# Optimization experiments

Measured on AMD Instinct MI355X. Metric: run time of the kernel, lower is better.

## Reference

```python
import jax, jax.numpy as jnp
import numpy as np

B, S, H, UNITS = 32, 2048, 1024, 1024


def setup_inputs() -> dict:
    key = jax.random.key(0)
    ks = jax.random.split(key, 5)
    scale = 1.0 / np.sqrt(H)
    return {
        "query": jax.random.normal(ks[0], (B, H), dtype=jnp.float32),
        "values": jax.random.normal(ks[1], (B, S, H), dtype=jnp.float32),
        "W1": jax.random.normal(ks[2], (H, UNITS), dtype=jnp.float32) * scale,
        "b1": jnp.zeros((UNITS,), dtype=jnp.float32),
        "W2": jax.random.normal(ks[3], (H, UNITS), dtype=jnp.float32) * scale,
        "b2": jnp.zeros((UNITS,), dtype=jnp.float32),
        "V": jax.random.normal(ks[4], (UNITS, 1), dtype=jnp.float32) * (1.0 / np.sqrt(UNITS)),
        "bV": jnp.zeros((1,), dtype=jnp.float32),
    }


def reference(query, values, W1, b1, W2, b2, V, bV):
    # W1(values): [B,S,U]; W2(query): [B,1,U] broadcast over S
    proj_v = jnp.einsum("bsh,hu->bsu", values, W1) + b1
    proj_q = (query @ W2 + b2)[:, None, :]
    score = jnp.tanh(proj_v + proj_q) @ V + bV          # [B,S,1]
    attention_weights = jax.nn.softmax(score, axis=1)   # softmax over seq
    context_vector = jnp.sum(attention_weights * values, axis=1)  # [B,H]
    return (attention_weights, context_vector)
```

## Files before the change

### kernel.cpp

```cpp
#include <hip/hip_runtime.h>
#include <hip/hip_bf16.h>
#include <stdint.h>

#define B_ 32
#define S_ 2048
#define H_ 1024
#define U_ 1024

typedef __attribute__((ext_vector_type(8))) short short8;
typedef __attribute__((ext_vector_type(4))) float f32x4;

#define AS1 __attribute__((address_space(1)))
#define AS3 __attribute__((address_space(3)))
#define FENCE __builtin_amdgcn_sched_barrier(0)

__device__ __forceinline__ unsigned short f2bf(float f) {
  unsigned int u = __float_as_uint(f);
  u += 0x7fffu + ((u >> 16) & 1u);
  return (unsigned short)(u >> 16);
}

__global__ void k_transpose_w1(const float* __restrict__ W1, unsigned short* __restrict__ W1T) {
  __shared__ float tile[64][65];
  const int tx = threadIdx.x, ty = threadIdx.y;
  const int u0 = blockIdx.x * 64, h0 = blockIdx.y * 64;
#pragma unroll
  for (int i = 0; i < 16; ++i) {
    int hl = ty + i * 4;
    tile[hl][tx] = W1[(size_t)(h0 + hl) * U_ + (u0 + tx)];
  }
  __syncthreads();
#pragma unroll
  for (int i = 0; i < 16; ++i) {
    int ul = ty + i * 4;
    W1T[(size_t)(u0 + ul) * H_ + (h0 + tx)] = f2bf(tile[tx][ul]);
  }
}

__global__ void k_b1q_part(const float* __restrict__ query, const float* __restrict__ W2,
                           float* __restrict__ qpart) {
  __shared__ float q_sh[32 * 128];
  const int u = blockIdx.x * 256 + threadIdx.x;
  const int hs = blockIdx.y;
  for (int i = threadIdx.x; i < 4096; i += 256) {
    const int b = i >> 7, h = i & 127;
    q_sh[i] = query[b * H_ + hs * 128 + h];
  }
  __syncthreads();
  float acc[32];
#pragma unroll
  for (int b = 0; b < 32; ++b) acc[b] = 0.f;
  for (int h = 0; h < 128; ++h) {
    const float w = W2[(size_t)(hs * 128 + h) * U_ + u];
#pragma unroll
    for (int b = 0; b < 32; ++b) acc[b] += q_sh[b * 128 + h] * w;
  }
#pragma unroll
  for (int b = 0; b < 32; ++b) qpart[((size_t)hs * 32 + b) * U_ + u] = acc[b];
}

__global__ void k_b1q_comb(const float* __restrict__ qpart, const float* __restrict__ b1,
                           const float* __restrict__ b2, float* __restrict__ b1q) {
  const int u = blockIdx.x * 256 + threadIdx.x;
  const int b = blockIdx.y;
  float s = b1[u] + b2[u];
#pragma unroll
  for (int hs = 0; hs < 8; ++hs) s += qpart[((size_t)hs * 32 + b) * U_ + u];
  b1q[b * U_ + u] = s;
}

#define BM 128
#define BN 256
#define BK 32
#define NSTEP 32

__global__ __launch_bounds__(512, 4)
void k_fused_score(const float* __restrict__ values,
                   const unsigned short* __restrict__ W1T,
                   const float* __restrict__ b1q, const float* __restrict__ V,
                   float* __restrict__ score_part) {
  __shared__ __align__(16) unsigned char smem[65536];
  unsigned short* As = (unsigned short*)smem;
  unsigned short* Bs = (unsigned short*)(smem + 16384);
  float* scorebuf = (float*)smem;

  const int tid = threadIdx.x;
  const int g = blockIdx.x;
  const int seq = (g & 7) * 256 + (g >> 3);
  const int bn = seq & 3;
  const int bm = seq >> 2;

  const int lane = tid & 63, wid = tid >> 6;
  const int wm = wid >> 2, wn = wid & 3;
  const int u0 = bn * BN;

  const int arow = tid >> 2;
  const int alc  = tid & 3;
  const int aplc = alc ^ ((arow >> 1) & 3);
  const float* aSrcF = values + (size_t)(bm * BM + arow) * H_ + alc * 8;
  const int awoff = arow * 32 + aplc * 8;

  const int blc = (tid & 3) ^ ((arow >> 1) & 3);
  const unsigned short* bSrc0 = W1T + (size_t)(u0 + arow) * H_ + blc * 8;
  const unsigned short* bSrc1 = bSrc0 + (size_t)128 * H_;

  const int l15 = lane & 15, l16 = lane >> 4;
  const int fsq = ((l16 ^ ((lane >> 1) & 3)) << 3);
  const int pA = (wm * 64 + l15) * 32 + fsq;
  const int pB = (wn * 64 + l15) * 32 + fsq;

  f32x4 acc[4][4];
#pragma unroll
  for (int mf = 0; mf < 4; ++mf)
#pragma unroll
    for (int nf = 0; nf < 4; ++nf) acc[mf][nf] = (f32x4){0.f, 0.f, 0.f, 0.f};

  float4 ar0, ar1;

#define ISSUE_ARF(tt) { \
    const float4* p_ = (const float4*)(aSrcF + (tt) * BK); \
    ar0 = p_[0]; ar1 = p_[1]; }

#define WRITE_ARF(slot) { \
    short8 w_; \
    w_[0]=f2bf(ar0.x); w_[1]=f2bf(ar0.y); w_[2]=f2bf(ar0.z); w_[3]=f2bf(ar0.w); \
    w_[4]=f2bf(ar1.x); w_[5]=f2bf(ar1.y); w_[6]=f2bf(ar1.z); w_[7]=f2bf(ar1.w); \
    *(short8*)&As[(slot) * 4096 + awoff] = w_; }

#define STAGE_B(tt, slot) { \
    const int ko_ = (tt) * BK; \
    __builtin_amdgcn_global_load_lds((const AS1 void*)(bSrc0 + ko_), \
        (AS3 void*)&Bs[(slot) * 8192 + tid * 8], 16, 0, 0); \
    __builtin_amdgcn_global_load_lds((const AS1 void*)(bSrc1 + ko_), \
        (AS3 void*)&Bs[(slot) * 8192 + 4096 + tid * 8], 16, 0, 0); }

  ISSUE_ARF(0);
  STAGE_B(0, 0);
  STAGE_B(1, 1);
  asm volatile("s_waitcnt vmcnt(4)" ::: "memory");
  WRITE_ARF(0);
  asm volatile("s_waitcnt vmcnt(2)" ::: "memory");
  asm volatile("s_waitcnt lgkmcnt(0)" ::: "memory");
  FENCE;
  __builtin_amdgcn_s_barrier();

  for (int t = 0; t < NSTEP; ++t) {
    const int aslot = t & 1;
    const int bslot = t % 3;
    if (t + 1 < NSTEP) { ISSUE_ARF(t + 1); }
    if (t + 2 < NSTEP) { STAGE_B(t + 2, (t + 2) % 3); }
    FENCE;
    short8 af[4], bv[4];
#pragma unroll
    for (int mf = 0; mf < 4; ++mf)
      af[mf] = *(const short8*)&As[aslot * 4096 + pA + mf * 512];
#pragma unroll
    for (int nf = 0; nf < 4; ++nf)
      bv[nf] = *(const short8*)&Bs[bslot * 8192 + pB + nf * 512];
#pragma unroll
    for (int nf = 0; nf < 4; ++nf)
#pragma unroll
      for (int mf = 0; mf < 4; ++mf)
        acc[mf][nf] = __builtin_amdgcn_mfma_f32_16x16x32_bf16(af[mf], bv[nf], acc[mf][nf], 0, 0, 0);
    FENCE;
    if (t + 2 < NSTEP)      { asm volatile("s_waitcnt vmcnt(2)" ::: "memory"); }
    else                    { asm volatile("s_waitcnt vmcnt(0)" ::: "memory"); }
    if (t + 1 < NSTEP) { WRITE_ARF((t + 1) & 1); }
    asm volatile("s_waitcnt lgkmcnt(0)" ::: "memory");
    FENCE;
    __builtin_amdgcn_s_barrier();
  }

  __syncthreads();
  const int b_blk = bm >> 4;
  float bqv[4], vvv[4];
#pragma unroll
  for (int nf = 0; nf < 4; ++nf) {
    const int ug = u0 + wn * 64 + nf * 16 + l15;
    bqv[nf] = b1q[b_blk * U_ + ug];
    vvv[nf] = V[ug];
  }
  float rp[4][4];
#pragma unroll
  for (int mf = 0; mf < 4; ++mf)
#pragma unroll
    for (int j = 0; j < 4; ++j) rp[mf][j] = 0.f;
#pragma unroll
  for (int nf = 0; nf < 4; ++nf)
#pragma unroll
    for (int mf = 0; mf < 4; ++mf) {
      const f32x4 c = acc[mf][nf];
#pragma unroll
      for (int j = 0; j < 4; ++j) {
        const float x = c[j] + bqv[nf];
        const float e = __expf(2.f * x);
        const float tt = 1.f - 2.f / (e + 1.f);
        rp[mf][j] += tt * vvv[nf];
      }
    }
#pragma unroll
  for (int mf = 0; mf < 4; ++mf)
#pragma unroll
    for (int j = 0; j < 4; ++j) {
      float v = rp[mf][j];
      v += __shfl_xor(v, 1);
      v += __shfl_xor(v, 2);
      v += __shfl_xor(v, 4);
      v += __shfl_xor(v, 8);
      rp[mf][j] = v;
    }
  if (l15 == 0) {
#pragma unroll
    for (int mf = 0; mf < 4; ++mf)
#pragma unroll
      for (int j = 0; j < 4; ++j)
        scorebuf[(wm * 64 + mf * 16 + l16 * 4 + j) * 4 + wn] = rp[mf][j];
  }
  __syncthreads();
  if (tid < BM) {
    const float s = scorebuf[tid * 4 + 0] + scorebuf[tid * 4 + 1] +
                    scorebuf[tid * 4 + 2] + scorebuf[tid * 4 + 3];
    score_part[(size_t)bn * (B_ * S_) + bm * BM + tid] = s;
  }
}

__global__ void k_softmax(const float* __restrict__ sp, float* __restrict__ aw) {
  __shared__ float red[8];
  const int b = blockIdx.x, tid = threadIdx.x;
  const int BS = B_ * S_;
  float x[8];
  float m = -1e30f;
#pragma unroll
  for (int i = 0; i < 8; ++i) {
    const int s = b * S_ + tid + i * 256;
    x[i] = sp[s] + sp[BS + s] + sp[2 * BS + s] + sp[3 * BS + s];
    m = fmaxf(m, x[i]);
  }
#pragma unroll
  for (int off = 32; off; off >>= 1) m = fmaxf(m, __shfl_xor(m, off));
  if ((tid & 63) == 0) red[tid >> 6] = m;
  __syncthreads();
  m = fmaxf(fmaxf(red[0], red[1]), fmaxf(red[2], red[3]));
  float e[8];
  float sum = 0.f;
#pragma unroll
  for (int i = 0; i < 8; ++i) { e[i] = __expf(x[i] - m); sum += e[i]; }
#pragma unroll
  for (int off = 32; off; off >>= 1) sum += __shfl_xor(sum, off);
  __syncthreads();
  if ((tid & 63) == 0) red[4 + (tid >> 6)] = sum;
  __syncthreads();
  sum = red[4] + red[5] + red[6] + red[7];
  const float inv = 1.f / sum;
#pragma unroll
  for (int i = 0; i < 8; ++i) aw[b * S_ + tid + i * 256] = e[i] * inv;
}

__global__ void k_ctx_partial(const float* __restrict__ values, const float* __restrict__ aw,
                              float* __restrict__ part) {
  __shared__ float a_s[64];
  const int b = blockIdx.y, sc = blockIdx.x, tid = threadIdx.x;
  if (tid < 64) a_s[tid] = aw[b * S_ + sc * 64 + tid];
  __syncthreads();
  const float4* vp = (const float4*)values + (size_t)(b * S_ + sc * 64) * (H_ / 4) + tid;
  float4 acc = {0.f, 0.f, 0.f, 0.f};
#pragma unroll 4
  for (int i = 0; i < 64; ++i) {
    const float4 v = vp[(size_t)i * (H_ / 4)];
    const float a = a_s[i];
    acc.x += a * v.x; acc.y += a * v.y; acc.z += a * v.z; acc.w += a * v.w;
  }
  ((float4*)part)[(size_t)(b * 32 + sc) * (H_ / 4) + tid] = acc;
}

__global__ void k_ctx_combine(const float* __restrict__ part, float* __restrict__ ctx) {
  const int b = blockIdx.x, tid = threadIdx.x;
  float4 s = {0.f, 0.f, 0.f, 0.f};
#pragma unroll
  for (int c = 0; c < 32; ++c) {
    const float4 v = ((const float4*)part)[(size_t)(b * 32 + c) * (H_ / 4) + tid];
    s.x += v.x; s.y += v.y; s.z += v.z; s.w += v.w;
  }
  ((float4*)ctx)[b * (H_ / 4) + tid] = s;
}

extern "C" void kernel_launch(void* const* d_in, const int* in_sizes, int n_in,
                              void* d_out, int out_size, void* d_ws, size_t ws_size,
                              hipStream_t stream) {
  const float* query  = (const float*)d_in[0];
  const float* values = (const float*)d_in[1];
  const float* W1     = (const float*)d_in[2];
  const float* b1     = (const float*)d_in[3];
  const float* W2     = (const float*)d_in[4];
  const float* b2     = (const float*)d_in[5];
  const float* V      = (const float*)d_in[6];

  char* ws = (char*)d_ws;
  unsigned short* W1T = (unsigned short*)ws;
  float* b1q   = (float*)(ws + 2u * 1024u * 1024u);
  float* spart = (float*)(ws + 2u * 1024u * 1024u + 128u * 1024u);
  float* qpart = (float*)(ws + 3u * 1024u * 1024u + 128u * 1024u);
  float* cpart = (float*)(ws + 4u * 1024u * 1024u + 256u * 1024u);

  float* aw  = (float*)d_out;
  float* ctx = aw + B_ * S_;

  k_transpose_w1<<<dim3(16, 16), dim3(64, 4), 0, stream>>>(W1, W1T);
  k_b1q_part<<<dim3(4, 8), dim3(256), 0, stream>>>(query, W2, qpart);
  k_b1q_comb<<<dim3(4, 32), dim3(256), 0, stream>>>(qpart, b1, b2, b1q);
  k_fused_score<<<dim3(2048), dim3(512), 0, stream>>>(values, W1T, b1q, V, spart);
  k_softmax<<<dim3(32), dim3(256), 0, stream>>>(spart, aw);
  k_ctx_partial<<<dim3(32, 32), dim3(256), 0, stream>>>(values, aw, cpart);
  k_ctx_combine<<<dim3(32), dim3(256), 0, stream>>>(cpart, ctx);
}
```

Baseline: 285.4 us.

## Stage fp32 A tiles via async global_load_lds and convert to bf16 after LDS read

Loading of the values operand changes. Before, threads loaded fp32 values into registers, converted them to bf16 and wrote them to LDS. Now raw fp32 tiles go straight to LDS through asynchronous global_load_lds, with an XOR swizzle, and each wave converts to bf16 after reading its fragments. This removes the register staging and the separate conversion/LDS-write step from the critical path, and lets A loads overlap like the B loads. In exchange LDS use grows to 80KB, and each A element is converted once per N-wave (4x redundant VALU work).

```diff
diff --git a/kernel.cpp b/kernel.cpp
--- a/kernel.cpp
+++ b/kernel.cpp
@@ -79,9 +79,9 @@
                    const unsigned short* __restrict__ W1T,
                    const float* __restrict__ b1q, const float* __restrict__ V,
                    float* __restrict__ score_part) {
-  __shared__ __align__(16) unsigned char smem[65536];
-  unsigned short* As = (unsigned short*)smem;
-  unsigned short* Bs = (unsigned short*)(smem + 16384);
+  __shared__ __align__(16) unsigned char smem[81920];
+  float* Af = (float*)smem;
+  unsigned short* Bs = (unsigned short*)(smem + 32768);
   float* scorebuf = (float*)smem;
 
   const int tid = threadIdx.x;
@@ -94,19 +94,21 @@
   const int wm = wid >> 2, wn = wid & 3;
   const int u0 = bn * BN;
 
-  const int arow = tid >> 2;
-  const int alc  = tid & 3;
-  const int aplc = alc ^ ((arow >> 1) & 3);
-  const float* aSrcF = values + (size_t)(bm * BM + arow) * H_ + alc * 8;
-  const int awoff = arow * 32 + aplc * 8;
-
-  const int blc = (tid & 3) ^ ((arow >> 1) & 3);
-  const unsigned short* bSrc0 = W1T + (size_t)(u0 + arow) * H_ + blc * 8;
-  const unsigned short* bSrc1 = bSrc0 + (size_t)128 * H_;
+  const int ar8 = tid >> 3;
+  const int lcA = (tid & 7) ^ (ar8 & 7);
+  const float* pafA = values + (size_t)(bm * BM + ar8) * H_ + lcA * 4;
+  const float* pafB = pafA + (size_t)64 * H_;
+
+  const int ar4 = tid >> 2;
+  const int blc = (tid & 3) ^ ((ar4 >> 1) & 3);
+  const unsigned short* pb0 = W1T + (size_t)(u0 + ar4) * H_ + blc * 8;
+  const unsigned short* pb1 = pb0 + (size_t)128 * H_;
 
   const int l15 = lane & 15, l16 = lane >> 4;
+  const int s7 = l15 & 7;
+  const int pAf0 = (wm * 64 + l15) * 32 + ((2 * l16)     ^ s7) * 4;
+  const int pAf1 = (wm * 64 + l15) * 32 + ((2 * l16 + 1) ^ s7) * 4;
   const int fsq = ((l16 ^ ((lane >> 1) & 3)) << 3);
-  const int pA = (wm * 64 + l15) * 32 + fsq;
   const int pB = (wn * 64 + l15) * 32 + fsq;
 
   f32x4 acc[4][4];
@@ -115,58 +117,51 @@
 #pragma unroll
     for (int nf = 0; nf < 4; ++nf) acc[mf][nf] = (f32x4){0.f, 0.f, 0.f, 0.f};
 
-  float4 ar0, ar1;
-
-#define ISSUE_ARF(tt) { \
-    const float4* p_ = (const float4*)(aSrcF + (tt) * BK); \
-    ar0 = p_[0]; ar1 = p_[1]; }
-
-#define WRITE_ARF(slot) { \
-    short8 w_; \
-    w_[0]=f2bf(ar0.x); w_[1]=f2bf(ar0.y); w_[2]=f2bf(ar0.z); w_[3]=f2bf(ar0.w); \
-    w_[4]=f2bf(ar1.x); w_[5]=f2bf(ar1.y); w_[6]=f2bf(ar1.z); w_[7]=f2bf(ar1.w); \
-    *(short8*)&As[(slot) * 4096 + awoff] = w_; }
-
-#define STAGE_B(tt, slot) { \
-    const int ko_ = (tt) * BK; \
-    __builtin_amdgcn_global_load_lds((const AS1 void*)(bSrc0 + ko_), \
-        (AS3 void*)&Bs[(slot) * 8192 + tid * 8], 16, 0, 0); \
-    __builtin_amdgcn_global_load_lds((const AS1 void*)(bSrc1 + ko_), \
-        (AS3 void*)&Bs[(slot) * 8192 + 4096 + tid * 8], 16, 0, 0); }
-
-  ISSUE_ARF(0);
-  STAGE_B(0, 0);
-  STAGE_B(1, 1);
-  asm volatile("s_waitcnt vmcnt(4)" ::: "memory");
-  WRITE_ARF(0);
+#define STAGE_A(tt) { \
+    const int sl_ = ((tt) & 1) * 4096; \
+    __builtin_amdgcn_global_load_lds((const AS1 void*)(pafA + (size_t)(tt) * BK), \
+        (AS3 void*)&Af[sl_ + tid * 4], 16, 0, 0); \
+    __builtin_amdgcn_global_load_lds((const AS1 void*)(pafB + (size_t)(tt) * BK), \
+        (AS3 void*)&Af[sl_ + 2048 + tid * 4], 16, 0, 0); }
+
+#define STAGE_B(tt) { \
+    const int sl_ = ((tt) % 3) * 8192; \
+    __builtin_amdgcn_global_load_lds((const AS1 void*)(pb0 + (size_t)(tt) * BK), \
+        (AS3 void*)&Bs[sl_ + tid * 8], 16, 0, 0); \
+    __builtin_amdgcn_global_load_lds((const AS1 void*)(pb1 + (size_t)(tt) * BK), \
+        (AS3 void*)&Bs[sl_ + 4096 + tid * 8], 16, 0, 0); }
+
+  STAGE_A(0);
+  STAGE_B(0);
+  STAGE_B(1);
   asm volatile("s_waitcnt vmcnt(2)" ::: "memory");
-  asm volatile("s_waitcnt lgkmcnt(0)" ::: "memory");
   FENCE;
   __builtin_amdgcn_s_barrier();
 
   for (int t = 0; t < NSTEP; ++t) {
-    const int aslot = t & 1;
-    const int bslot = t % 3;
-    if (t + 1 < NSTEP) { ISSUE_ARF(t + 1); }
-    if (t + 2 < NSTEP) { STAGE_B(t + 2, (t + 2) % 3); }
+    if (t + 1 < NSTEP) STAGE_A(t + 1);
+    if (t + 2 < NSTEP) STAGE_B(t + 2);
     FENCE;
-    short8 af[4], bv[4];
-#pragma unroll
-    for (int mf = 0; mf < 4; ++mf)
-      af[mf] = *(const short8*)&As[aslot * 4096 + pA + mf * 512];
+    const int aOff = (t & 1) * 4096;
+    const int bOff = (t % 3) * 8192;
+    short8 bv[4];
 #pragma unroll
     for (int nf = 0; nf < 4; ++nf)
-      bv[nf] = *(const short8*)&Bs[bslot * 8192 + pB + nf * 512];
-#pragma unroll
-    for (int nf = 0; nf < 4; ++nf)
-#pragma unroll
-      for (int mf = 0; mf < 4; ++mf)
-        acc[mf][nf] = __builtin_amdgcn_mfma_f32_16x16x32_bf16(af[mf], bv[nf], acc[mf][nf], 0, 0, 0);
+      bv[nf] = *(const short8*)&Bs[bOff + pB + nf * 512];
+#pragma unroll
+    for (int mf = 0; mf < 4; ++mf) {
+      const f32x4 a0 = *(const f32x4*)&Af[aOff + pAf0 + mf * 512];
+      const f32x4 a1 = *(const f32x4*)&Af[aOff + pAf1 + mf * 512];
+      short8 af;
+      af[0] = f2bf(a0[0]); af[1] = f2bf(a0[1]); af[2] = f2bf(a0[2]); af[3] = f2bf(a0[3]);
+      af[4] = f2bf(a1[0]); af[5] = f2bf(a1[1]); af[6] = f2bf(a1[2]); af[7] = f2bf(a1[3]);
+#pragma unroll
+      for (int nf = 0; nf < 4; ++nf)
+        acc[mf][nf] = __builtin_amdgcn_mfma_f32_16x16x32_bf16(af, bv[nf], acc[mf][nf], 0, 0, 0);
+    }
     FENCE;
-    if (t + 2 < NSTEP)      { asm volatile("s_waitcnt vmcnt(2)" ::: "memory"); }
-    else                    { asm volatile("s_waitcnt vmcnt(0)" ::: "memory"); }
-    if (t + 1 < NSTEP) { WRITE_ARF((t + 1) & 1); }
-    asm volatile("s_waitcnt lgkmcnt(0)" ::: "memory");
+    if (t + 2 < NSTEP) { asm volatile("s_waitcnt vmcnt(2)" ::: "memory"); }
+    else               { asm volatile("s_waitcnt vmcnt(0)" ::: "memory"); }
     FENCE;
     __builtin_amdgcn_s_barrier();
   }
```

Measured after the change: 310.8 us. 1.09x slower.
